# Kernel optimization log

Hardware: AMD Instinct MI355X
Metric: run time of the kernel (lower is better)

Reference implementation:

```python
import jax, jax.numpy as jnp
import numpy as np

B, S, D, H = 4, 1024, 1024, 16
DK = D // H
NEG = -1e9


def setup_inputs() -> dict:
    key = jax.random.key(0)
    ks = jax.random.split(key, 8)
    inp = {
        "query": jax.random.normal(ks[0], (B, S, D), dtype=jnp.float32),
        "key": jax.random.normal(ks[1], (B, S, D), dtype=jnp.float32),
        "value": jax.random.normal(ks[2], (B, S, D), dtype=jnp.float32),
        "mask": jax.random.randint(ks[3], (B, S, S), 0, 2, dtype=jnp.int32),
        # bias-free Linear weights, torch layout [out, in]; y = x @ W.T
        "Wq": jax.random.normal(ks[4], (D, D), dtype=jnp.float32) / np.sqrt(D),
        "Wk": jax.random.normal(ks[5], (D, D), dtype=jnp.float32) / np.sqrt(D),
        "Wv": jax.random.normal(ks[6], (D, D), dtype=jnp.float32) / np.sqrt(D),
        "Wo": jax.random.normal(ks[7], (D, D), dtype=jnp.float32) / np.sqrt(D),
    }
    return inp


def _split_heads(x):
    # [B, S, D] -> [B, H, S, DK]
    return x.reshape(B, -1, H, DK).transpose(0, 2, 1, 3)


def reference(query, key, value, mask, Wq, Wk, Wv, Wo):
    q = _split_heads(query @ Wq.T)
    k = _split_heads(key @ Wk.T)
    v = _split_heads(value @ Wv.T)
    scores = jnp.einsum("bhqd,bhkd->bhqk", q, k) / jnp.sqrt(jnp.float32(DK))
    scores = jnp.where(mask[:, None, :, :] == 0, NEG, scores)
    p_attn = jax.nn.softmax(scores, axis=-1)
    x = jnp.einsum("bhqk,bhkd->bhqd", p_attn, v)
    x = x.transpose(0, 2, 1, 3).reshape(B, -1, D)
    # dropout p=0.0 (eval-equivalent): identity
    return x @ Wo.T
```

## Files before the change

### kernel.cpp

```cpp
#include <hip/hip_runtime.h>

#define BB 4
#define SS 1024
#define DD 1024
#define HH 16
#define DKK 64
#define MM (BB*SS)

typedef __bf16 bf16;
typedef __bf16 bf16x8 __attribute__((ext_vector_type(8)));
typedef float f32x4 __attribute__((ext_vector_type(4)));
typedef float f32x16 __attribute__((ext_vector_type(16)));

__device__ __forceinline__ f32x4 mfma16(bf16x8 a, bf16x8 b, f32x4 c) {
  return __builtin_amdgcn_mfma_f32_16x16x32_bf16(a, b, c, 0, 0, 0);
}
__device__ __forceinline__ f32x16 mfma32(bf16x8 a, bf16x8 b, f32x16 c) {
  return __builtin_amdgcn_mfma_f32_32x32x16_bf16(a, b, c, 0, 0, 0);
}
__device__ __forceinline__ float fexp2(float x) {
  return __builtin_amdgcn_exp2f(x);
}
__device__ __forceinline__ void gld_lds16(const bf16* g, bf16* l) {
  __builtin_amdgcn_global_load_lds(
      (const __attribute__((address_space(1))) void*)g,
      (__attribute__((address_space(3))) void*)l, 16, 0, 0);
}

__global__ __launch_bounds__(256)
void k_cvt7(const float* __restrict__ s0, const float* __restrict__ s1,
            const float* __restrict__ s2, const float* __restrict__ s3,
            const float* __restrict__ s4, const float* __restrict__ s5,
            const float* __restrict__ s6,
            bf16* __restrict__ d0, bf16* __restrict__ d1, bf16* __restrict__ d2,
            bf16* __restrict__ d3, bf16* __restrict__ d4, bf16* __restrict__ d5,
            bf16* __restrict__ d6) {
  const int t = blockIdx.y;
  const float* s = (t == 0) ? s0 : (t == 1) ? s1 : (t == 2) ? s2
                 : (t == 3) ? s3 : (t == 4) ? s4 : (t == 5) ? s5 : s6;
  bf16* d = (t == 0) ? d0 : (t == 1) ? d1 : (t == 2) ? d2
          : (t == 3) ? d3 : (t == 4) ? d4 : (t == 5) ? d5 : d6;
  const int n = (t < 3) ? (MM * DD) : (DD * DD);
  const int i0 = (blockIdx.x * 256 + threadIdx.x) * 8;
  if (i0 >= n) return;
  const f32x4 a = *(const f32x4*)(s + i0);
  const f32x4 b = *(const f32x4*)(s + i0 + 4);
  bf16x8 o;
#pragma unroll
  for (int j = 0; j < 4; ++j) { o[j] = (bf16)a[j]; o[4 + j] = (bf16)b[j]; }
  *(bf16x8*)(d + i0) = o;
}

__global__ __launch_bounds__(256) void k_mask_bits(const int* __restrict__ mask,
                                                   unsigned* __restrict__ bits) {
  const int row = blockIdx.x;
  const int tid = threadIdx.x;
  const int lane = tid & 63, wv = tid >> 6;
#pragma unroll
  for (int it = 0; it < 4; ++it) {
    const int base = it * 256 + wv * 64;
    const int col = base + lane;
    unsigned long long bal = __ballot(mask[(size_t)row * SS + col] != 0);
    if (lane == 0) {
      bits[(size_t)row * 32 + (base >> 5)] = (unsigned)bal;
      bits[(size_t)row * 32 + (base >> 5) + 1] = (unsigned)(bal >> 32);
    }
  }
}

#define QSCALE 0.1803368801111204f

template<int AF32, int CF32>
__device__ __forceinline__ void gemm_body(const void* __restrict__ Ap,
                                          const float* __restrict__ Wp,
                                          void* __restrict__ Cp,
                                          int Mtot, int N, int K, int blk,
                                          float oscale) {
  __shared__ bf16 Al[128 * 40];
  __shared__ bf16 Bl[128 * 40];
  const int tid = threadIdx.x;
  const int lane = tid & 63;
  const int l15 = lane & 15, l4 = lane >> 4;
  const int wv = tid >> 6;
  const int nbm = Mtot >> 7;
  const int bm = blk % nbm, bn = blk / nbm;
  const size_t m0 = (size_t)bm << 7, n0 = (size_t)bn << 7;
  const int wr = (wv >> 1) << 6, wc = (wv & 1) << 6;
  const int srow = tid >> 2, scol = (tid & 3) << 3;

  f32x4 acc[4][4];
#pragma unroll
  for (int i = 0; i < 4; ++i)
#pragma unroll
    for (int j = 0; j < 4; ++j) acc[i][j] = f32x4{0.f, 0.f, 0.f, 0.f};

  for (int k0 = 0; k0 < K; k0 += 32) {
#pragma unroll
    for (int c = 0; c < 2; ++c) {
      const int row = (c << 6) + srow;
      bf16x8 av;
      if (AF32) {
        const float* s = (const float*)Ap + (m0 + row) * (size_t)K + k0 + scol;
        f32x4 v0 = *(const f32x4*)s;
        f32x4 v1 = *(const f32x4*)(s + 4);
#pragma unroll
        for (int j = 0; j < 4; ++j) { av[j] = (bf16)v0[j]; av[4 + j] = (bf16)v1[j]; }
      } else {
        av = *(const bf16x8*)((const bf16*)Ap + (m0 + row) * (size_t)K + k0 + scol);
      }
      *(bf16x8*)&Al[row * 40 + scol] = av;

      const float* ws_ = Wp + (n0 + row) * (size_t)K + k0 + scol;
      f32x4 w0 = *(const f32x4*)ws_;
      f32x4 w1 = *(const f32x4*)(ws_ + 4);
      bf16x8 wv8;
#pragma unroll
      for (int j = 0; j < 4; ++j) { wv8[j] = (bf16)w0[j]; wv8[4 + j] = (bf16)w1[j]; }
      *(bf16x8*)&Bl[row * 40 + scol] = wv8;
    }
    __syncthreads();

    bf16x8 af[4], bfv[4];
#pragma unroll
    for (int t = 0; t < 4; ++t) {
      af[t]  = *(const bf16x8*)&Al[(wr + t * 16 + l15) * 40 + l4 * 8];
      bfv[t] = *(const bf16x8*)&Bl[(wc + t * 16 + l15) * 40 + l4 * 8];
    }
    __builtin_amdgcn_s_setprio(1);
#pragma unroll
    for (int mt = 0; mt < 4; ++mt)
#pragma unroll
      for (int nt = 0; nt < 4; ++nt)
        acc[mt][nt] = mfma16(af[mt], bfv[nt], acc[mt][nt]);
    __builtin_amdgcn_s_setprio(0);
    __syncthreads();
  }

#pragma unroll
  for (int mt = 0; mt < 4; ++mt)
#pragma unroll
    for (int nt = 0; nt < 4; ++nt)
#pragma unroll
      for (int r = 0; r < 4; ++r) {
        const size_t row = m0 + wr + mt * 16 + l4 * 4 + r;
        const size_t col = n0 + wc + nt * 16 + l15;
        if (CF32) ((float*)Cp)[row * N + col] = acc[mt][nt][r];
        else      ((bf16*)Cp)[row * N + col] = (bf16)(acc[mt][nt][r] * oscale);
      }
}

__global__ __launch_bounds__(256)
void k_gemm_qkv(const float* __restrict__ A0, const float* __restrict__ A1,
                const float* __restrict__ A2, const float* __restrict__ W0,
                const float* __restrict__ W1, const float* __restrict__ W2,
                bf16* __restrict__ C0, bf16* __restrict__ C1, bf16* __restrict__ C2) {
  const int z = blockIdx.z;
  const float* A = (z == 0) ? A0 : (z == 1) ? A1 : A2;
  const float* W = (z == 0) ? W0 : (z == 1) ? W1 : W2;
  bf16* C = (z == 0) ? C0 : (z == 1) ? C1 : C2;
  const float sc = (z == 0) ? QSCALE : 1.0f;
  gemm_body<1, 0>(A, W, C, MM, DD, DD, blockIdx.x, sc);
}

__global__ __launch_bounds__(256)
void k_gemm_out(const bf16* __restrict__ A, const float* __restrict__ W,
                float* __restrict__ C) {
  gemm_body<0, 1>(A, W, C, MM, DD, DD, blockIdx.x, 1.0f);
}

__global__ __launch_bounds__(256)
void k_gemm_qkv_b16(const bf16* __restrict__ A0, const bf16* __restrict__ A1,
                    const bf16* __restrict__ A2, const bf16* __restrict__ W0,
                    const bf16* __restrict__ W1, const bf16* __restrict__ W2,
                    bf16* __restrict__ C0, bf16* __restrict__ C1,
                    bf16* __restrict__ C2) {
  __shared__ bf16 Al[128 * 32];
  __shared__ bf16 Bl[128 * 32];
  const int z = blockIdx.z;
  const bf16* A = (z == 0) ? A0 : (z == 1) ? A1 : A2;
  const bf16* W = (z == 0) ? W0 : (z == 1) ? W1 : W2;
  bf16* C = (z == 0) ? C0 : (z == 1) ? C1 : C2;
  const float oscale = (z == 0) ? QSCALE : 1.0f;

  const int tid = threadIdx.x, lane = tid & 63, w = tid >> 6;
  const int l15 = lane & 15, l4 = lane >> 4;
  const int bm = blockIdx.x & 31, bn = blockIdx.x >> 5;
  const size_t m0 = (size_t)bm << 7, n0 = (size_t)bn << 7;
  const int wr = (w >> 1) << 6, wc = (w & 1) << 6;
  const int srow = w * 32 + (lane >> 2);
  const int scol = (lane & 3) << 3;

  f32x4 acc[4][4];
#pragma unroll
  for (int i = 0; i < 4; ++i)
#pragma unroll
    for (int j = 0; j < 4; ++j) acc[i][j] = f32x4{0.f, 0.f, 0.f, 0.f};

  for (int k0 = 0; k0 < DD; k0 += 32) {
    const bf16* ga = A + (m0 + srow) * (size_t)DD + k0 + scol;
    const bf16* gb = W + (n0 + srow) * (size_t)DD + k0 + scol;
    gld_lds16(ga,            &Al[(w * 32) * 32]);
    gld_lds16(ga + 16 * DD,  &Al[(w * 32 + 16) * 32]);
    gld_lds16(gb,            &Bl[(w * 32) * 32]);
    gld_lds16(gb + 16 * DD,  &Bl[(w * 32 + 16) * 32]);
    __syncthreads();

    bf16x8 af[4], bfv[4];
#pragma unroll
    for (int t = 0; t < 4; ++t) {
      af[t]  = *(const bf16x8*)&Al[(wr + t * 16 + l15) * 32 + l4 * 8];
      bfv[t] = *(const bf16x8*)&Bl[(wc + t * 16 + l15) * 32 + l4 * 8];
    }
#pragma unroll
    for (int mt = 0; mt < 4; ++mt)
#pragma unroll
      for (int nt = 0; nt < 4; ++nt)
        acc[mt][nt] = mfma16(af[mt], bfv[nt], acc[mt][nt]);
    __syncthreads();
  }

#pragma unroll
  for (int mt = 0; mt < 4; ++mt)
#pragma unroll
    for (int nt = 0; nt < 4; ++nt)
#pragma unroll
      for (int r = 0; r < 4; ++r) {
        const size_t row = m0 + wr + mt * 16 + l4 * 4 + r;
        const size_t col = n0 + wc + nt * 16 + l15;
        C[row * DD + col] = (bf16)(acc[mt][nt][r] * oscale);
      }
}

__global__ __launch_bounds__(256)
void k_gemm_out_b16(const bf16* __restrict__ A, const bf16* __restrict__ W,
                    float* __restrict__ C) {
  __shared__ bf16 Al[128 * 32];
  __shared__ bf16 Bl[128 * 32];
  const int tid = threadIdx.x, lane = tid & 63, w = tid >> 6;
  const int l15 = lane & 15, l4 = lane >> 4;
  const int bm = blockIdx.x & 31, bn = blockIdx.x >> 5;
  const size_t m0 = (size_t)bm << 7, n0 = (size_t)bn << 7;
  const int wr = (w >> 1) << 6, wc = (w & 1) << 6;
  const int srow = w * 32 + (lane >> 2);
  const int scol = (lane & 3) << 3;

  f32x4 acc[4][4];
#pragma unroll
  for (int i = 0; i < 4; ++i)
#pragma unroll
    for (int j = 0; j < 4; ++j) acc[i][j] = f32x4{0.f, 0.f, 0.f, 0.f};

  for (int k0 = 0; k0 < DD; k0 += 32) {
    const bf16* ga = A + (m0 + srow) * (size_t)DD + k0 + scol;
    const bf16* gb = W + (n0 + srow) * (size_t)DD + k0 + scol;
    gld_lds16(ga,            &Al[(w * 32) * 32]);
    gld_lds16(ga + 16 * DD,  &Al[(w * 32 + 16) * 32]);
    gld_lds16(gb,            &Bl[(w * 32) * 32]);
    gld_lds16(gb + 16 * DD,  &Bl[(w * 32 + 16) * 32]);
    __syncthreads();

    bf16x8 af[4], bfv[4];
#pragma unroll
    for (int t = 0; t < 4; ++t) {
      af[t]  = *(const bf16x8*)&Al[(wr + t * 16 + l15) * 32 + l4 * 8];
      bfv[t] = *(const bf16x8*)&Bl[(wc + t * 16 + l15) * 32 + l4 * 8];
    }
#pragma unroll
    for (int mt = 0; mt < 4; ++mt)
#pragma unroll
      for (int nt = 0; nt < 4; ++nt)
        acc[mt][nt] = mfma16(af[mt], bfv[nt], acc[mt][nt]);
    __syncthreads();
  }

#pragma unroll
  for (int mt = 0; mt < 4; ++mt)
#pragma unroll
    for (int nt = 0; nt < 4; ++nt)
#pragma unroll
      for (int r = 0; r < 4; ++r) {
        const size_t row = m0 + wr + mt * 16 + l4 * 4 + r;
        const size_t col = n0 + wc + nt * 16 + l15;
        C[row * DD + col] = acc[mt][nt][r];
      }
}

#define VKS 34
__global__ __launch_bounds__(256)
void k_attn(const bf16* __restrict__ Qw, const bf16* __restrict__ Kw,
            const bf16* __restrict__ Vw, const unsigned* __restrict__ mb,
            bf16* __restrict__ Xw) {
  __shared__ union {
    bf16 v[4][64 * VKS];
    struct { float o[32 * 66]; float ml[4][2][32];
             float inv[32]; float mst[32]; } m;
  } sh;
  const int tid = threadIdx.x, lane = tid & 63, w = tid >> 6;
  const int l31 = lane & 31, hi = lane >> 5;
  const int l15 = lane & 15, g = lane >> 4;
  const unsigned bid = blockIdx.x;
  const unsigned wg = (bid & 7) * 256 + (bid >> 3);
  const int bh = wg >> 5, qt = wg & 31;
  const int h = bh & 15, b = bh >> 4;
  const int q0 = qt * 32;

  bf16x8 qf[4];
  {
    const bf16* Qb = Qw + (size_t)(b * SS + q0 + l31) * DD + h * 64 + hi * 8;
#pragma unroll
    for (int kt = 0; kt < 4; ++kt) qf[kt] = *(const bf16x8*)(Qb + kt * 16);
  }
  const bf16* Kb = Kw + (size_t)(b * SS) * DD + h * 64 + hi * 8;
  const bf16* Vbp = Vw + (size_t)(b * SS) * DD + h * 64 + l15 * 4;
  const unsigned* mrow = mb + (size_t)(b * SS + q0 + l31) * 32 + w * 8;

  f32x16 acco[2];
#pragma unroll
  for (int dt = 0; dt < 2; ++dt)
#pragma unroll
    for (int r = 0; r < 16; ++r) acco[dt][r] = 0.f;
  float mx = -3e38f, ssum = 0.f;

  bf16* Vl = sh.v[w];
  const int kvw = w << 8;

  for (int it = 0; it < 8; ++it) {
    const int kv0 = kvw + it * 32;
    union { uint2 u; bf16 h4[4]; } vld[8];
#pragma unroll
    for (int i = 0; i < 8; ++i)
      vld[i].u = *(const uint2*)(Vbp + (size_t)(kv0 + i * 4 + g) * DD);
    bf16x8 kf[4];
    {
      const bf16* kp = Kb + (size_t)(kv0 + l31) * DD;
#pragma unroll
      for (int kt = 0; kt < 4; ++kt) kf[kt] = *(const bf16x8*)(kp + kt * 16);
    }
    const unsigned mw = mrow[it];
#pragma unroll
    for (int i = 0; i < 8; ++i)
#pragma unroll
      for (int j = 0; j < 4; ++j)
        Vl[(l15 * 4 + j) * VKS + i * 4 + g] = vld[i].h4[j];

    f32x16 s;
#pragma unroll
    for (int r = 0; r < 16; ++r) s[r] = 0.f;
    __builtin_amdgcn_s_setprio(1);
#pragma unroll
    for (int kt = 0; kt < 4; ++kt) s = mfma32(kf[kt], qf[kt], s);
    __builtin_amdgcn_s_setprio(0);

    float p[16];
#pragma unroll
    for (int r = 0; r < 16; ++r) {
      const int pos = (r & 3) + 8 * (r >> 2) + 4 * hi;
      p[r] = ((mw >> pos) & 1) ? s[r] : -1e9f;
    }
    float rm = p[0];
#pragma unroll
    for (int r = 1; r < 16; ++r) rm = fmaxf(rm, p[r]);
    rm = fmaxf(rm, __shfl_xor(rm, 32));
    if (!__all(rm <= mx + 8.0f)) {
      const float mn = fmaxf(mx, rm);
      const float scal = fexp2(mx - mn);
      mx = mn; ssum *= scal;
      float sr[16];
#pragma unroll
      for (int r = 0; r < 16; ++r)
        sr[r] = __shfl(scal, (r & 3) + 8 * (r >> 2) + 4 * hi);
#pragma unroll
      for (int dt = 0; dt < 2; ++dt)
#pragma unroll
        for (int r = 0; r < 16; ++r) acco[dt][r] *= sr[r];
    }
#pragma unroll
    for (int r = 0; r < 16; ++r) { p[r] = fexp2(p[r] - mx); ssum += p[r]; }

    int dpk[8];
#pragma unroll
    for (int i = 0; i < 8; ++i) {
      union { bf16 hh[2]; int v; } u;
      u.hh[0] = (bf16)p[2 * i]; u.hh[1] = (bf16)p[2 * i + 1];
      dpk[i] = u.v;
    }
    const int sa = hi ? dpk[0] : dpk[2], sb = hi ? dpk[1] : dpk[3];
    const int sc_ = hi ? dpk[4] : dpk[6], sd = hi ? dpk[5] : dpk[7];
    const int ra = __shfl_xor(sa, 32), rb = __shfl_xor(sb, 32);
    const int rc = __shfl_xor(sc_, 32), rd = __shfl_xor(sd, 32);
    union { bf16x8 v; int q[4]; } pa0, pa1;
    pa0.q[0] = hi ? ra : dpk[0];  pa0.q[1] = hi ? rb : dpk[1];
    pa0.q[2] = hi ? dpk[2] : ra;  pa0.q[3] = hi ? dpk[3] : rb;
    pa1.q[0] = hi ? rc : dpk[4];  pa1.q[1] = hi ? rd : dpk[5];
    pa1.q[2] = hi ? dpk[6] : rc;  pa1.q[3] = hi ? dpk[7] : rd;

    __builtin_amdgcn_s_setprio(1);
#pragma unroll
    for (int dt = 0; dt < 2; ++dt) {
      const bf16* vp = &Vl[(dt * 32 + l31) * VKS + 8 * hi];
      bf16x8 v0 = *(const bf16x8*)vp;
      bf16x8 v1 = *(const bf16x8*)(vp + 16);
      acco[dt] = mfma32(pa0.v, v0, acco[dt]);
      acco[dt] = mfma32(pa1.v, v1, acco[dt]);
    }
    __builtin_amdgcn_s_setprio(0);
  }

  ssum += __shfl_xor(ssum, 32);
  __syncthreads();
  if (hi == 0) { sh.m.ml[w][0][l31] = mx; sh.m.ml[w][1][l31] = ssum; }
  __syncthreads();
  if (w == 0 && hi == 0) {
    const float M0 = sh.m.ml[0][0][l31], M1 = sh.m.ml[1][0][l31];
    const float M2 = sh.m.ml[2][0][l31], M3 = sh.m.ml[3][0][l31];
    const float ms = fmaxf(fmaxf(M0, M1), fmaxf(M2, M3));
    const float ls = sh.m.ml[0][1][l31] * fexp2(M0 - ms)
                   + sh.m.ml[1][1][l31] * fexp2(M1 - ms)
                   + sh.m.ml[2][1][l31] * fexp2(M2 - ms)
                   + sh.m.ml[3][1][l31] * fexp2(M3 - ms);
    sh.m.inv[l31] = 1.0f / ls;
    sh.m.mst[l31] = ms;
  }
  __syncthreads();
  float fown[16];
#pragma unroll
  for (int r = 0; r < 16; ++r) {
    const int q_ = (r & 3) + 8 * (r >> 2) + 4 * hi;
    fown[r] = fexp2(sh.m.ml[w][0][q_] - sh.m.mst[q_]);
  }
  for (int rd2 = 0; rd2 < 4; ++rd2) {
    if (w == rd2) {
#pragma unroll
      for (int dt = 0; dt < 2; ++dt)
#pragma unroll
        for (int r = 0; r < 16; ++r) {
          const int q_ = (r & 3) + 8 * (r >> 2) + 4 * hi;
          const int o = q_ * 66 + dt * 32 + l31;
          const float val = acco[dt][r] * fown[r];
          if (rd2 == 0) sh.m.o[o] = val;
          else          sh.m.o[o] += val;
        }
    }
    __syncthreads();
  }
  {
    const int row = tid >> 3, c0 = (tid & 7) * 8;
    const float inv = sh.m.inv[row];
    const float* orow = &sh.m.o[row * 66 + c0];
    bf16x8 ov;
#pragma unroll
    for (int j = 0; j < 8; ++j) ov[j] = (bf16)(orow[j] * inv);
    *(bf16x8*)(Xw + (size_t)(b * SS + q0 + row) * DD + h * 64 + c0) = ov;
  }
}

extern "C" void kernel_launch(void* const* d_in, const int* in_sizes, int n_in,
                              void* d_out, int out_size, void* d_ws, size_t ws_size,
                              hipStream_t stream) {
  const float* q32 = (const float*)d_in[0];
  const float* k32 = (const float*)d_in[1];
  const float* v32 = (const float*)d_in[2];
  const int* mask = (const int*)d_in[3];
  const float* Wq = (const float*)d_in[4];
  const float* Wk = (const float*)d_in[5];
  const float* Wv = (const float*)d_in[6];
  const float* Wo = (const float*)d_in[7];
  float* out = (float*)d_out;

  const size_t eAct = (size_t)MM * DD;
  const size_t eW = (size_t)DD * DD;

  bf16* Qb = (bf16*)d_ws;
  bf16* Kb = Qb + eAct;
  bf16* Vb = Kb + eAct;
  bf16* Xb = Vb + eAct;
  unsigned* mbits = (unsigned*)(Xb + eAct);
  bf16* cvtBase = (bf16*)(mbits + (size_t)MM * 32);
  bf16* Aq = cvtBase;
  bf16* Ak = Aq + eAct;
  bf16* Av = Ak + eAct;
  bf16* Wqb = Av + eAct;
  bf16* Wkb = Wqb + eW;
  bf16* Wvb = Wkb + eW;
  bf16* Wob = Wvb + eW;
  const size_t need = (size_t)((bf16*)(Wob + eW) - (bf16*)d_ws) * sizeof(bf16);

  k_mask_bits<<<BB * SS, 256, 0, stream>>>(mask, mbits);
  if (ws_size >= need) {
    k_cvt7<<<dim3(2048, 7), 256, 0, stream>>>(q32, k32, v32, Wq, Wk, Wv, Wo,
                                              Aq, Ak, Av, Wqb, Wkb, Wvb, Wob);
    k_gemm_qkv_b16<<<dim3(256, 1, 3), 256, 0, stream>>>(
        Aq, Ak, Av, Wqb, Wkb, Wvb, Qb, Kb, Vb);
    k_attn<<<BB * HH * (SS / 32), 256, 0, stream>>>(Qb, Kb, Vb, mbits, Xb);
    k_gemm_out_b16<<<256, 256, 0, stream>>>(Xb, Wob, out);
  } else {
    k_gemm_qkv<<<dim3((MM / 128) * (DD / 128), 1, 3), 256, 0, stream>>>(
        q32, k32, v32, Wq, Wk, Wv, Qb, Kb, Vb);
    k_attn<<<BB * HH * (SS / 32), 256, 0, stream>>>(Qb, Kb, Vb, mbits, Xb);
    k_gemm_out<<<(MM / 128) * (DD / 128), 256, 0, stream>>>(Xb, Wo, out);
  }
}
```

Before: 148.2 us.

## Pre-transpose V per head so attention loads MFMA operands directly from global

Adds a separate kernel that transposes V into a per-(batch,head) [64, S] layout. The attention kernel then loads the PV MFMA B operands straight from global memory as contiguous bf16x8 vectors. This removes the per-iteration LDS scatter-transpose of V and the LDS reads in the inner loop. The row max and row sum reductions are also rewritten as balanced trees to shorten dependency chains. The cost is an extra kernel launch plus an extra write and read of V. The fallback path now writes the transpose buffer without the workspace size check.

```diff
diff --git a/kernel.cpp b/kernel.cpp
--- a/kernel.cpp
+++ b/kernel.cpp
@@ -68,6 +68,30 @@
   }
 }
 
+__global__ __launch_bounds__(256)
+void k_vt(const bf16* __restrict__ V, bf16* __restrict__ Vt) {
+  __shared__ bf16 t[64 * 65];
+  const int st = blockIdx.x, h = blockIdx.y, b = blockIdx.z;
+  const int row = threadIdx.x >> 3;
+  const int c0 = (threadIdx.x & 7) * 8;
+#pragma unroll
+  for (int half = 0; half < 2; ++half) {
+    const int s = row + half * 32;
+    bf16x8 v = *(const bf16x8*)(V + (size_t)(b * SS + st * 64 + s) * DD + h * 64 + c0);
+#pragma unroll
+    for (int j = 0; j < 8; ++j) t[s * 65 + c0 + j] = v[j];
+  }
+  __syncthreads();
+#pragma unroll
+  for (int half = 0; half < 2; ++half) {
+    const int d = row + half * 32;
+    bf16x8 o;
+#pragma unroll
+    for (int j = 0; j < 8; ++j) o[j] = t[(c0 + j) * 65 + d];
+    *(bf16x8*)(Vt + (size_t)((b * HH + h) * 64 + d) * SS + st * 64 + c0) = o;
+  }
+}
+
 #define QSCALE 0.1803368801111204f
 
 template<int AF32, int CF32>
@@ -285,19 +309,14 @@
       }
 }
 
-#define VKS 34
 __global__ __launch_bounds__(256)
 void k_attn(const bf16* __restrict__ Qw, const bf16* __restrict__ Kw,
-            const bf16* __restrict__ Vw, const unsigned* __restrict__ mb,
+            const bf16* __restrict__ Vt, const unsigned* __restrict__ mb,
             bf16* __restrict__ Xw) {
-  __shared__ union {
-    bf16 v[4][64 * VKS];
-    struct { float o[32 * 66]; float ml[4][2][32];
-             float inv[32]; float mst[32]; } m;
-  } sh;
+  __shared__ struct { float o[32 * 66]; float ml[4][2][32];
+                      float inv[32]; float mst[32]; } sh;
   const int tid = threadIdx.x, lane = tid & 63, w = tid >> 6;
   const int l31 = lane & 31, hi = lane >> 5;
-  const int l15 = lane & 15, g = lane >> 4;
   const unsigned bid = blockIdx.x;
   const unsigned wg = (bid & 7) * 256 + (bid >> 3);
   const int bh = wg >> 5, qt = wg & 31;
@@ -311,7 +330,7 @@
     for (int kt = 0; kt < 4; ++kt) qf[kt] = *(const bf16x8*)(Qb + kt * 16);
   }
   const bf16* Kb = Kw + (size_t)(b * SS) * DD + h * 64 + hi * 8;
-  const bf16* Vbp = Vw + (size_t)(b * SS) * DD + h * 64 + l15 * 4;
+  const bf16* Vtb = Vt + (size_t)(b * HH + h) * 64 * SS;
   const unsigned* mrow = mb + (size_t)(b * SS + q0 + l31) * 32 + w * 8;
 
   f32x16 acco[2];
@@ -320,28 +339,24 @@
 #pragma unroll
     for (int r = 0; r < 16; ++r) acco[dt][r] = 0.f;
   float mx = -3e38f, ssum = 0.f;
-
-  bf16* Vl = sh.v[w];
   const int kvw = w << 8;
 
   for (int it = 0; it < 8; ++it) {
     const int kv0 = kvw + it * 32;
-    union { uint2 u; bf16 h4[4]; } vld[8];
-#pragma unroll
-    for (int i = 0; i < 8; ++i)
-      vld[i].u = *(const uint2*)(Vbp + (size_t)(kv0 + i * 4 + g) * DD);
     bf16x8 kf[4];
     {
       const bf16* kp = Kb + (size_t)(kv0 + l31) * DD;
 #pragma unroll
       for (int kt = 0; kt < 4; ++kt) kf[kt] = *(const bf16x8*)(kp + kt * 16);
     }
+    bf16x8 vf[2][2];
+#pragma unroll
+    for (int dt = 0; dt < 2; ++dt) {
+      const bf16* vp = Vtb + (size_t)(dt * 32 + l31) * SS + kv0 + hi * 8;
+      vf[dt][0] = *(const bf16x8*)vp;
+      vf[dt][1] = *(const bf16x8*)(vp + 16);
+    }
     const unsigned mw = mrow[it];
-#pragma unroll
-    for (int i = 0; i < 8; ++i)
-#pragma unroll
-      for (int j = 0; j < 4; ++j)
-        Vl[(l15 * 4 + j) * VKS + i * 4 + g] = vld[i].h4[j];
 
     f32x16 s;
 #pragma unroll
@@ -357,9 +372,12 @@
       const int pos = (r & 3) + 8 * (r >> 2) + 4 * hi;
       p[r] = ((mw >> pos) & 1) ? s[r] : -1e9f;
     }
-    float rm = p[0];
-#pragma unroll
-    for (int r = 1; r < 16; ++r) rm = fmaxf(rm, p[r]);
+    float t0 = fmaxf(p[0], p[1]),  t1 = fmaxf(p[2], p[3]);
+    float t2 = fmaxf(p[4], p[5]),  t3 = fmaxf(p[6], p[7]);
+    float t4 = fmaxf(p[8], p[9]),  t5 = fmaxf(p[10], p[11]);
+    float t6 = fmaxf(p[12], p[13]), t7 = fmaxf(p[14], p[15]);
+    float rm = fmaxf(fmaxf(fmaxf(t0, t1), fmaxf(t2, t3)),
+                     fmaxf(fmaxf(t4, t5), fmaxf(t6, t7)));
     rm = fmaxf(rm, __shfl_xor(rm, 32));
     if (!__all(rm <= mx + 8.0f)) {
       const float mn = fmaxf(mx, rm);
@@ -375,7 +393,14 @@
         for (int r = 0; r < 16; ++r) acco[dt][r] *= sr[r];
     }
 #pragma unroll
-    for (int r = 0; r < 16; ++r) { p[r] = fexp2(p[r] - mx); ssum += p[r]; }
+    for (int r = 0; r < 16; ++r) p[r] = fexp2(p[r] - mx);
+    {
+      float a0 = (p[0] + p[1]) + (p[2] + p[3]);
+      float a1 = (p[4] + p[5]) + (p[6] + p[7]);
+      float a2 = (p[8] + p[9]) + (p[10] + p[11]);
+      float a3 = (p[12] + p[13]) + (p[14] + p[15]);
+      ssum += (a0 + a1) + (a2 + a3);
+    }
 
     int dpk[8];
 #pragma unroll
@@ -397,36 +422,33 @@
     __builtin_amdgcn_s_setprio(1);
 #pragma unroll
     for (int dt = 0; dt < 2; ++dt) {
-      const bf16* vp = &Vl[(dt * 32 + l31) * VKS + 8 * hi];
-      bf16x8 v0 = *(const bf16x8*)vp;
-      bf16x8 v1 = *(const bf16x8*)(vp + 16);
-      acco[dt] = mfma32(pa0.v, v0, acco[dt]);
-      acco[dt] = mfma32(pa1.v, v1, acco[dt]);
+      acco[dt] = mfma32(pa0.v, vf[dt][0], acco[dt]);
+      acco[dt] = mfma32(pa1.v, vf[dt][1], acco[dt]);
     }
     __builtin_amdgcn_s_setprio(0);
   }
 
   ssum += __shfl_xor(ssum, 32);
   __syncthreads();
-  if (hi == 0) { sh.m.ml[w][0][l31] = mx; sh.m.ml[w][1][l31] = ssum; }
+  if (hi == 0) { sh.ml[w][0][l31] = mx; sh.ml[w][1][l31] = ssum; }
   __syncthreads();
   if (w == 0 && hi == 0) {
-    const float M0 = sh.m.ml[0][0][l31], M1 = sh.m.ml[1][0][l31];
-    const float M2 = sh.m.ml[2][0][l31], M3 = sh.m.ml[3][0][l31];
+    const float M0 = sh.ml[0][0][l31], M1 = sh.ml[1][0][l31];
+    const float M2 = sh.ml[2][0][l31], M3 = sh.ml[3][0][l31];
     const float ms = fmaxf(fmaxf(M0, M1), fmaxf(M2, M3));
-    const float ls = sh.m.ml[0][1][l31] * fexp2(M0 - ms)
-                   + sh.m.ml[1][1][l31] * fexp2(M1 - ms)
-                   + sh.m.ml[2][1][l31] * fexp2(M2 - ms)
-                   + sh.m.ml[3][1][l31] * fexp2(M3 - ms);
-    sh.m.inv[l31] = 1.0f / ls;
-    sh.m.mst[l31] = ms;
+    const float ls = sh.ml[0][1][l31] * fexp2(M0 - ms)
+                   + sh.ml[1][1][l31] * fexp2(M1 - ms)
+                   + sh.ml[2][1][l31] * fexp2(M2 - ms)
+                   + sh.ml[3][1][l31] * fexp2(M3 - ms);
+    sh.inv[l31] = 1.0f / ls;
+    sh.mst[l31] = ms;
   }
   __syncthreads();
   float fown[16];
 #pragma unroll
   for (int r = 0; r < 16; ++r) {
     const int q_ = (r & 3) + 8 * (r >> 2) + 4 * hi;
-    fown[r] = fexp2(sh.m.ml[w][0][q_] - sh.m.mst[q_]);
+    fown[r] = fexp2(sh.ml[w][0][q_] - sh.mst[q_]);
   }
   for (int rd2 = 0; rd2 < 4; ++rd2) {
     if (w == rd2) {
@@ -437,16 +459,16 @@
           const int q_ = (r & 3) + 8 * (r >> 2) + 4 * hi;
           const int o = q_ * 66 + dt * 32 + l31;
           const float val = acco[dt][r] * fown[r];
-          if (rd2 == 0) sh.m.o[o] = val;
-          else          sh.m.o[o] += val;
+          if (rd2 == 0) sh.o[o] = val;
+          else          sh.o[o] += val;
         }
     }
     __syncthreads();
   }
   {
     const int row = tid >> 3, c0 = (tid & 7) * 8;
-    const float inv = sh.m.inv[row];
-    const float* orow = &sh.m.o[row * 66 + c0];
+    const float inv = sh.inv[row];
+    const float* orow = &sh.o[row * 66 + c0];
     bf16x8 ov;
 #pragma unroll
     for (int j = 0; j < 8; ++j) ov[j] = (bf16)(orow[j] * inv);
@@ -475,7 +497,8 @@
   bf16* Vb = Kb + eAct;
   bf16* Xb = Vb + eAct;
   unsigned* mbits = (unsigned*)(Xb + eAct);
-  bf16* cvtBase = (bf16*)(mbits + (size_t)MM * 32);
+  bf16* Vtp = (bf16*)(mbits + (size_t)MM * 32);
+  bf16* cvtBase = Vtp + eAct;
   bf16* Aq = cvtBase;
   bf16* Ak = Aq + eAct;
   bf16* Av = Ak + eAct;
@@ -491,12 +514,14 @@
                                               Aq, Ak, Av, Wqb, Wkb, Wvb, Wob);
     k_gemm_qkv_b16<<<dim3(256, 1, 3), 256, 0, stream>>>(
         Aq, Ak, Av, Wqb, Wkb, Wvb, Qb, Kb, Vb);
-    k_attn<<<BB * HH * (SS / 32), 256, 0, stream>>>(Qb, Kb, Vb, mbits, Xb);
+    k_vt<<<dim3(16, 16, 4), 256, 0, stream>>>(Vb, Vtp);
+    k_attn<<<BB * HH * (SS / 32), 256, 0, stream>>>(Qb, Kb, Vtp, mbits, Xb);
     k_gemm_out_b16<<<256, 256, 0, stream>>>(Xb, Wob, out);
   } else {
     k_gemm_qkv<<<dim3((MM / 128) * (DD / 128), 1, 3), 256, 0, stream>>>(
         q32, k32, v32, Wq, Wk, Wv, Qb, Kb, Vb);
-    k_attn<<<BB * HH * (SS / 32), 256, 0, stream>>>(Qb, Kb, Vb, mbits, Xb);
+    k_vt<<<dim3(16, 16, 4), 256, 0, stream>>>(Vb, Vtp);
+    k_attn<<<BB * HH * (SS / 32), 256, 0, stream>>>(Qb, Kb, Vtp, mbits, Xb);
     k_gemm_out<<<(MM / 128) * (DD / 128), 256, 0, stream>>>(Xb, Wo, out);
   }
 }
```

Result: slower. 166.2 us (+12.2%).

## Process 64 queries per attention block with double-buffered async K/V LDS loads

Applied to the files above, without the earlier changes.

The attention kernel now handles two 32-query tiles per workgroup, so each K/V tile loaded is reused across 64 queries and the grid is halved. K and V are copied into LDS with asynchronous global-to-LDS loads, double-buffered with explicit vmcnt waits, and K uses an XOR swizzle to avoid bank conflicts. V is read transposed from LDS, and the PV MFMA operand order is swapped so the rescale becomes a per-lane scalar. The cost is more registers (two accumulator sets) and fewer blocks in flight, which may reduce occupancy.

```diff
diff --git a/kernel.cpp b/kernel.cpp
--- a/kernel.cpp
+++ b/kernel.cpp
@@ -285,172 +285,223 @@
       }
 }
 
-#define VKS 34
 __global__ __launch_bounds__(256)
 void k_attn(const bf16* __restrict__ Qw, const bf16* __restrict__ Kw,
             const bf16* __restrict__ Vw, const unsigned* __restrict__ mb,
             bf16* __restrict__ Xw) {
   __shared__ union {
-    bf16 v[4][64 * VKS];
-    struct { float o[32 * 66]; float ml[4][2][32];
-             float inv[32]; float mst[32]; } m;
+    struct { bf16 k[2][2048]; bf16 v[2][2048]; } st[4];
+    struct { float o[64 * 67]; float ml[4][2][64];
+             float inv[64]; float mst[64]; } m;
   } sh;
   const int tid = threadIdx.x, lane = tid & 63, w = tid >> 6;
   const int l31 = lane & 31, hi = lane >> 5;
-  const int l15 = lane & 15, g = lane >> 4;
   const unsigned bid = blockIdx.x;
-  const unsigned wg = (bid & 7) * 256 + (bid >> 3);
-  const int bh = wg >> 5, qt = wg & 31;
+  const unsigned wg = (bid & 7) * 128 + (bid >> 3);
+  const int bh = wg >> 4, qblk = wg & 15;
   const int h = bh & 15, b = bh >> 4;
-  const int q0 = qt * 32;
-
-  bf16x8 qf[4];
-  {
-    const bf16* Qb = Qw + (size_t)(b * SS + q0 + l31) * DD + h * 64 + hi * 8;
-#pragma unroll
-    for (int kt = 0; kt < 4; ++kt) qf[kt] = *(const bf16x8*)(Qb + kt * 16);
-  }
-  const bf16* Kb = Kw + (size_t)(b * SS) * DD + h * 64 + hi * 8;
-  const bf16* Vbp = Vw + (size_t)(b * SS) * DD + h * 64 + l15 * 4;
-  const unsigned* mrow = mb + (size_t)(b * SS + q0 + l31) * 32 + w * 8;
-
-  f32x16 acco[2];
-#pragma unroll
-  for (int dt = 0; dt < 2; ++dt)
-#pragma unroll
-    for (int r = 0; r < 16; ++r) acco[dt][r] = 0.f;
-  float mx = -3e38f, ssum = 0.f;
-
-  bf16* Vl = sh.v[w];
+  const int q0 = qblk * 64;
+
+  bf16x8 qf[2][4];
+#pragma unroll
+  for (int qt = 0; qt < 2; ++qt) {
+    const bf16* Qb = Qw + (size_t)(b * SS + q0 + qt * 32 + l31) * DD + h * 64 + hi * 8;
+#pragma unroll
+    for (int kt = 0; kt < 4; ++kt) qf[qt][kt] = *(const bf16x8*)(Qb + kt * 16);
+  }
+  const bf16* Kg = Kw + (size_t)(b * SS) * DD + h * 64;
+  const bf16* Vg = Vw + (size_t)(b * SS) * DD + h * 64;
+  const unsigned* mrow0 = mb + (size_t)(b * SS + q0 + l31) * 32 + w * 8;
+  const unsigned* mrow1 = mrow0 + 32 * 32;
+
+  const int grow = lane >> 3;
+  const int chV = (lane & 7) * 8;
+  const int chK = ((lane & 7) ^ grow) * 8;
   const int kvw = w << 8;
 
-  for (int it = 0; it < 8; ++it) {
-    const int kv0 = kvw + it * 32;
-    union { uint2 u; bf16 h4[4]; } vld[8];
-#pragma unroll
-    for (int i = 0; i < 8; ++i)
-      vld[i].u = *(const uint2*)(Vbp + (size_t)(kv0 + i * 4 + g) * DD);
+  bf16* Kst[2] = { sh.st[w].k[0], sh.st[w].k[1] };
+  bf16* Vst[2] = { sh.st[w].v[0], sh.st[w].v[1] };
+
+#define AISSUE(T, BUF)                                                      \
+  do {                                                                      \
+    _Pragma("unroll")                                                       \
+    for (int i_ = 0; i_ < 4; ++i_) {                                        \
+      const size_t r_ = (size_t)(kvw + (T) * 32 + i_ * 8 + grow) * DD;      \
+      gld_lds16(Kg + r_ + chK, Kst[BUF] + i_ * 512);                        \
+      gld_lds16(Vg + r_ + chV, Vst[BUF] + i_ * 512);                        \
+    }                                                                       \
+  } while (0)
+
+  f32x16 aco[2][2];
+#pragma unroll
+  for (int qt = 0; qt < 2; ++qt)
+#pragma unroll
+    for (int dt = 0; dt < 2; ++dt)
+#pragma unroll
+      for (int r = 0; r < 16; ++r) aco[qt][dt][r] = 0.f;
+  float mx[2] = { -3e38f, -3e38f }, ssum[2] = { 0.f, 0.f };
+
+  AISSUE(0, 0);
+  unsigned mw0 = mrow0[0], mw1 = mrow1[0];
+
+#pragma unroll
+  for (int t = 0; t < 8; ++t) {
+    const int cur = t & 1;
+    unsigned nm0 = 0, nm1 = 0;
+    if (t < 7) {
+      AISSUE(t + 1, cur ^ 1);
+      nm0 = mrow0[t + 1]; nm1 = mrow1[t + 1];
+      asm volatile("s_waitcnt vmcnt(10)" ::: "memory");
+    } else {
+      asm volatile("s_waitcnt vmcnt(0)" ::: "memory");
+    }
+    __builtin_amdgcn_sched_barrier(0);
+
+    const bf16* Kc = Kst[cur];
     bf16x8 kf[4];
-    {
-      const bf16* kp = Kb + (size_t)(kv0 + l31) * DD;
-#pragma unroll
-      for (int kt = 0; kt < 4; ++kt) kf[kt] = *(const bf16x8*)(kp + kt * 16);
-    }
-    const unsigned mw = mrow[it];
-#pragma unroll
-    for (int i = 0; i < 8; ++i)
-#pragma unroll
-      for (int j = 0; j < 4; ++j)
-        Vl[(l15 * 4 + j) * VKS + i * 4 + g] = vld[i].h4[j];
-
-    f32x16 s;
-#pragma unroll
-    for (int r = 0; r < 16; ++r) s[r] = 0.f;
-    __builtin_amdgcn_s_setprio(1);
-#pragma unroll
-    for (int kt = 0; kt < 4; ++kt) s = mfma32(kf[kt], qf[kt], s);
-    __builtin_amdgcn_s_setprio(0);
-
-    float p[16];
-#pragma unroll
-    for (int r = 0; r < 16; ++r) {
-      const int pos = (r & 3) + 8 * (r >> 2) + 4 * hi;
-      p[r] = ((mw >> pos) & 1) ? s[r] : -1e9f;
-    }
-    float rm = p[0];
-#pragma unroll
-    for (int r = 1; r < 16; ++r) rm = fmaxf(rm, p[r]);
-    rm = fmaxf(rm, __shfl_xor(rm, 32));
-    if (!__all(rm <= mx + 8.0f)) {
-      const float mn = fmaxf(mx, rm);
-      const float scal = fexp2(mx - mn);
-      mx = mn; ssum *= scal;
-      float sr[16];
-#pragma unroll
-      for (int r = 0; r < 16; ++r)
-        sr[r] = __shfl(scal, (r & 3) + 8 * (r >> 2) + 4 * hi);
-#pragma unroll
-      for (int dt = 0; dt < 2; ++dt)
-#pragma unroll
-        for (int r = 0; r < 16; ++r) acco[dt][r] *= sr[r];
-    }
-#pragma unroll
-    for (int r = 0; r < 16; ++r) { p[r] = fexp2(p[r] - mx); ssum += p[r]; }
-
-    int dpk[8];
-#pragma unroll
-    for (int i = 0; i < 8; ++i) {
-      union { bf16 hh[2]; int v; } u;
-      u.hh[0] = (bf16)p[2 * i]; u.hh[1] = (bf16)p[2 * i + 1];
-      dpk[i] = u.v;
-    }
-    const int sa = hi ? dpk[0] : dpk[2], sb = hi ? dpk[1] : dpk[3];
-    const int sc_ = hi ? dpk[4] : dpk[6], sd = hi ? dpk[5] : dpk[7];
-    const int ra = __shfl_xor(sa, 32), rb = __shfl_xor(sb, 32);
-    const int rc = __shfl_xor(sc_, 32), rd = __shfl_xor(sd, 32);
-    union { bf16x8 v; int q[4]; } pa0, pa1;
-    pa0.q[0] = hi ? ra : dpk[0];  pa0.q[1] = hi ? rb : dpk[1];
-    pa0.q[2] = hi ? dpk[2] : ra;  pa0.q[3] = hi ? dpk[3] : rb;
-    pa1.q[0] = hi ? rc : dpk[4];  pa1.q[1] = hi ? rd : dpk[5];
-    pa1.q[2] = hi ? dpk[6] : rc;  pa1.q[3] = hi ? dpk[7] : rd;
-
-    __builtin_amdgcn_s_setprio(1);
-#pragma unroll
-    for (int dt = 0; dt < 2; ++dt) {
-      const bf16* vp = &Vl[(dt * 32 + l31) * VKS + 8 * hi];
-      bf16x8 v0 = *(const bf16x8*)vp;
-      bf16x8 v1 = *(const bf16x8*)(vp + 16);
-      acco[dt] = mfma32(pa0.v, v0, acco[dt]);
-      acco[dt] = mfma32(pa1.v, v1, acco[dt]);
-    }
-    __builtin_amdgcn_s_setprio(0);
-  }
-
-  ssum += __shfl_xor(ssum, 32);
+#pragma unroll
+    for (int kt = 0; kt < 4; ++kt)
+      kf[kt] = *(const bf16x8*)&Kc[l31 * 64 + (((kt * 2 + hi) ^ (l31 & 7)) * 8)];
+    const bf16* Vc = Vst[cur];
+    bf16x8 va[2][2];
+#pragma unroll
+    for (int dt = 0; dt < 2; ++dt)
+#pragma unroll
+      for (int s2 = 0; s2 < 2; ++s2) {
+        bf16x8 tv;
+#pragma unroll
+        for (int j = 0; j < 8; ++j)
+          tv[j] = Vc[(s2 * 16 + hi * 8 + j) * 64 + dt * 32 + l31];
+        va[dt][s2] = tv;
+      }
+
+#pragma unroll
+    for (int qt = 0; qt < 2; ++qt) {
+      f32x16 s;
+#pragma unroll
+      for (int r = 0; r < 16; ++r) s[r] = 0.f;
+      __builtin_amdgcn_s_setprio(1);
+#pragma unroll
+      for (int kt = 0; kt < 4; ++kt) s = mfma32(kf[kt], qf[qt][kt], s);
+      __builtin_amdgcn_s_setprio(0);
+
+      const unsigned mw = qt ? mw1 : mw0;
+      float p[16];
+#pragma unroll
+      for (int r = 0; r < 16; ++r) {
+        const int pos = (r & 3) + 8 * (r >> 2) + 4 * hi;
+        p[r] = ((mw >> pos) & 1) ? s[r] : -1e9f;
+      }
+      float t0 = fmaxf(p[0], p[1]),  t1 = fmaxf(p[2], p[3]);
+      float t2 = fmaxf(p[4], p[5]),  t3 = fmaxf(p[6], p[7]);
+      float t4 = fmaxf(p[8], p[9]),  t5 = fmaxf(p[10], p[11]);
+      float t6 = fmaxf(p[12], p[13]), t7 = fmaxf(p[14], p[15]);
+      float rm = fmaxf(fmaxf(fmaxf(t0, t1), fmaxf(t2, t3)),
+                       fmaxf(fmaxf(t4, t5), fmaxf(t6, t7)));
+      rm = fmaxf(rm, __shfl_xor(rm, 32));
+      if (!__all(rm <= mx[qt] + 8.0f)) {
+        const float mn = fmaxf(mx[qt], rm);
+        const float scal = fexp2(mx[qt] - mn);
+        mx[qt] = mn; ssum[qt] *= scal;
+#pragma unroll
+        for (int dt = 0; dt < 2; ++dt)
+#pragma unroll
+          for (int r = 0; r < 16; ++r) aco[qt][dt][r] *= scal;
+      }
+#pragma unroll
+      for (int r = 0; r < 16; ++r) p[r] = fexp2(p[r] - mx[qt]);
+      {
+        float a0 = (p[0] + p[1]) + (p[2] + p[3]);
+        float a1 = (p[4] + p[5]) + (p[6] + p[7]);
+        float a2 = (p[8] + p[9]) + (p[10] + p[11]);
+        float a3 = (p[12] + p[13]) + (p[14] + p[15]);
+        ssum[qt] += (a0 + a1) + (a2 + a3);
+      }
+      int dpk[8];
+#pragma unroll
+      for (int i = 0; i < 8; ++i) {
+        union { bf16 hh[2]; int v; } u;
+        u.hh[0] = (bf16)p[2 * i]; u.hh[1] = (bf16)p[2 * i + 1];
+        dpk[i] = u.v;
+      }
+      const int sa = hi ? dpk[0] : dpk[2], sb = hi ? dpk[1] : dpk[3];
+      const int sc_ = hi ? dpk[4] : dpk[6], sd = hi ? dpk[5] : dpk[7];
+      const int ra = __shfl_xor(sa, 32), rb = __shfl_xor(sb, 32);
+      const int rc = __shfl_xor(sc_, 32), rd = __shfl_xor(sd, 32);
+      union { bf16x8 v; int q[4]; } pa0, pa1;
+      pa0.q[0] = hi ? ra : dpk[0];  pa0.q[1] = hi ? rb : dpk[1];
+      pa0.q[2] = hi ? dpk[2] : ra;  pa0.q[3] = hi ? dpk[3] : rb;
+      pa1.q[0] = hi ? rc : dpk[4];  pa1.q[1] = hi ? rd : dpk[5];
+      pa1.q[2] = hi ? dpk[6] : rc;  pa1.q[3] = hi ? dpk[7] : rd;
+
+      __builtin_amdgcn_s_setprio(1);
+#pragma unroll
+      for (int dt = 0; dt < 2; ++dt) {
+        aco[qt][dt] = mfma32(va[dt][0], pa0.v, aco[qt][dt]);
+        aco[qt][dt] = mfma32(va[dt][1], pa1.v, aco[qt][dt]);
+      }
+      __builtin_amdgcn_s_setprio(0);
+    }
+    mw0 = nm0; mw1 = nm1;
+  }
+#undef AISSUE
+
+#pragma unroll
+  for (int qt = 0; qt < 2; ++qt) ssum[qt] += __shfl_xor(ssum[qt], 32);
   __syncthreads();
-  if (hi == 0) { sh.m.ml[w][0][l31] = mx; sh.m.ml[w][1][l31] = ssum; }
+  if (hi == 0) {
+#pragma unroll
+    for (int qt = 0; qt < 2; ++qt) {
+      sh.m.ml[w][0][qt * 32 + l31] = mx[qt];
+      sh.m.ml[w][1][qt * 32 + l31] = ssum[qt];
+    }
+  }
   __syncthreads();
-  if (w == 0 && hi == 0) {
-    const float M0 = sh.m.ml[0][0][l31], M1 = sh.m.ml[1][0][l31];
-    const float M2 = sh.m.ml[2][0][l31], M3 = sh.m.ml[3][0][l31];
+  if (w == 0) {
+    const float M0 = sh.m.ml[0][0][lane], M1 = sh.m.ml[1][0][lane];
+    const float M2 = sh.m.ml[2][0][lane], M3 = sh.m.ml[3][0][lane];
     const float ms = fmaxf(fmaxf(M0, M1), fmaxf(M2, M3));
-    const float ls = sh.m.ml[0][1][l31] * fexp2(M0 - ms)
-                   + sh.m.ml[1][1][l31] * fexp2(M1 - ms)
-                   + sh.m.ml[2][1][l31] * fexp2(M2 - ms)
-                   + sh.m.ml[3][1][l31] * fexp2(M3 - ms);
-    sh.m.inv[l31] = 1.0f / ls;
-    sh.m.mst[l31] = ms;
+    const float ls = sh.m.ml[0][1][lane] * fexp2(M0 - ms)
+                   + sh.m.ml[1][1][lane] * fexp2(M1 - ms)
+                   + sh.m.ml[2][1][lane] * fexp2(M2 - ms)
+                   + sh.m.ml[3][1][lane] * fexp2(M3 - ms);
+    sh.m.inv[lane] = 1.0f / ls;
+    sh.m.mst[lane] = ms;
   }
   __syncthreads();
-  float fown[16];
-#pragma unroll
-  for (int r = 0; r < 16; ++r) {
-    const int q_ = (r & 3) + 8 * (r >> 2) + 4 * hi;
-    fown[r] = fexp2(sh.m.ml[w][0][q_] - sh.m.mst[q_]);
-  }
+  float fown[2];
+#pragma unroll
+  for (int qt = 0; qt < 2; ++qt)
+    fown[qt] = fexp2(sh.m.ml[w][0][qt * 32 + l31] - sh.m.mst[qt * 32 + l31]);
   for (int rd2 = 0; rd2 < 4; ++rd2) {
     if (w == rd2) {
 #pragma unroll
-      for (int dt = 0; dt < 2; ++dt)
-#pragma unroll
-        for (int r = 0; r < 16; ++r) {
-          const int q_ = (r & 3) + 8 * (r >> 2) + 4 * hi;
-          const int o = q_ * 66 + dt * 32 + l31;
-          const float val = acco[dt][r] * fown[r];
-          if (rd2 == 0) sh.m.o[o] = val;
-          else          sh.m.o[o] += val;
-        }
+      for (int qt = 0; qt < 2; ++qt)
+#pragma unroll
+        for (int dt = 0; dt < 2; ++dt)
+#pragma unroll
+          for (int r = 0; r < 16; ++r) {
+            const int d = dt * 32 + (r & 3) + 8 * (r >> 2) + 4 * hi;
+            const int o = d * 67 + qt * 32 + l31;
+            const float val = aco[qt][dt][r] * fown[qt];
+            if (rd2 == 0) sh.m.o[o] = val;
+            else          sh.m.o[o] += val;
+          }
     }
     __syncthreads();
   }
   {
-    const int row = tid >> 3, c0 = (tid & 7) * 8;
-    const float inv = sh.m.inv[row];
-    const float* orow = &sh.m.o[row * 66 + c0];
-    bf16x8 ov;
-#pragma unroll
-    for (int j = 0; j < 8; ++j) ov[j] = (bf16)(orow[j] * inv);
-    *(bf16x8*)(Xw + (size_t)(b * SS + q0 + row) * DD + h * 64 + c0) = ov;
+    const int q = tid >> 2, c0 = (tid & 3) * 16;
+    const float inv = sh.m.inv[q];
+    bf16x8 w0, w1;
+#pragma unroll
+    for (int j = 0; j < 8; ++j) {
+      w0[j] = (bf16)(sh.m.o[(c0 + j) * 67 + q] * inv);
+      w1[j] = (bf16)(sh.m.o[(c0 + 8 + j) * 67 + q] * inv);
+    }
+    bf16* xp = Xw + (size_t)(b * SS + q0 + q) * DD + h * 64 + c0;
+    *(bf16x8*)xp = w0;
+    *(bf16x8*)(xp + 8) = w1;
   }
 }
 
@@ -491,12 +542,12 @@
                                               Aq, Ak, Av, Wqb, Wkb, Wvb, Wob);
     k_gemm_qkv_b16<<<dim3(256, 1, 3), 256, 0, stream>>>(
         Aq, Ak, Av, Wqb, Wkb, Wvb, Qb, Kb, Vb);
-    k_attn<<<BB * HH * (SS / 32), 256, 0, stream>>>(Qb, Kb, Vb, mbits, Xb);
+    k_attn<<<BB * HH * (SS / 64), 256, 0, stream>>>(Qb, Kb, Vb, mbits, Xb);
     k_gemm_out_b16<<<256, 256, 0, stream>>>(Xb, Wob, out);
   } else {
     k_gemm_qkv<<<dim3((MM / 128) * (DD / 128), 1, 3), 256, 0, stream>>>(
         q32, k32, v32, Wq, Wk, Wv, Qb, Kb, Vb);
-    k_attn<<<BB * HH * (SS / 32), 256, 0, stream>>>(Qb, Kb, Vb, mbits, Xb);
+    k_attn<<<BB * HH * (SS / 64), 256, 0, stream>>>(Qb, Kb, Vb, mbits, Xb);
     k_gemm_out<<<(MM / 128) * (DD / 128), 256, 0, stream>>>(Xb, Wo, out);
   }
 }
```

After: 157.5 us. 1.06x slower.
